# Kernel tuning notes

Hardware: AMD Instinct MI355X
Metric: run time of the kernel (lower is better)

## Reference

```python
import jax, jax.numpy as jnp
import numpy as np

NUM_HEADS = 16


def setup_inputs() -> dict:
    key = jax.random.key(0)
    ks = jax.random.split(key, 9)
    B, S, D = 2, 2048, 1024
    scale = 1.0 / np.sqrt(D)
    return {
        "hidden_states": jax.random.normal(ks[0], (B, S, D), dtype=jnp.float32),
        "Wq": jax.random.normal(ks[1], (D, D), dtype=jnp.float32) * scale,
        "bq": jnp.zeros((D,), dtype=jnp.float32),
        "Wk": jax.random.normal(ks[2], (D, D), dtype=jnp.float32) * scale,
        "bk": jnp.zeros((D,), dtype=jnp.float32),
        "Wv": jax.random.normal(ks[3], (D, D), dtype=jnp.float32) * scale,
        "bv": jnp.zeros((D,), dtype=jnp.float32),
        "Wo": jax.random.normal(ks[4], (D, D), dtype=jnp.float32) * scale,
        "bo": jnp.zeros((D,), dtype=jnp.float32),
    }


def reference(hidden_states, Wq, bq, Wk, bk, Wv, bv, Wo, bo):
    B, S, D = hidden_states.shape
    H = NUM_HEADS
    hd = D // H
    # q/k/v projections (torch Linear uses x @ W.T + b)
    q = hidden_states @ Wq.T + bq
    k = hidden_states @ Wk.T + bk
    v = hidden_states @ Wv.T + bv
    # split heads: b s (h d) -> b h s d
    q = q.reshape(B, S, H, hd)
    k = k.reshape(B, S, H, hd)
    v = v.reshape(B, S, H, hd)
    # scaled dot-product attention (non-causal, no mask)
    scale = 1.0 / jnp.sqrt(jnp.asarray(hd, dtype=q.dtype))
    scores = jnp.einsum("bqhd,bkhd->bhqk", q, k) * scale
    probs = jax.nn.softmax(scores, axis=-1)
    attn = jnp.einsum("bhqk,bkhd->bqhd", probs, v)
    # merge heads and output projection
    attn = attn.reshape(B, S, D)
    return attn @ Wo.T + bo
```

## Files before the change

### kernel.cpp

```cpp
#include <hip/hip_runtime.h>

typedef short bf16x8 __attribute__((ext_vector_type(8)));
typedef short bf16x4 __attribute__((ext_vector_type(4)));
typedef float f32x4 __attribute__((ext_vector_type(4)));
typedef float float4v __attribute__((ext_vector_type(4)));
typedef unsigned short u16x8 __attribute__((ext_vector_type(8)));
typedef unsigned short u16x4 __attribute__((ext_vector_type(4)));

#define GLL16(g, l_) __builtin_amdgcn_global_load_lds( \
    (const __attribute__((address_space(1))) unsigned int*)(g), \
    (__attribute__((address_space(3))) unsigned int*)(l_), 16, 0, 0)

__device__ __forceinline__ unsigned short f2bf(float x) {
  unsigned u = __float_as_uint(x);
  u += 0x7fff + ((u >> 16) & 1);
  return (unsigned short)(u >> 16);
}

__device__ __forceinline__ unsigned cvtpk_bf16(float a, float b) {
  unsigned r;
  asm("v_cvt_pk_bf16_f32 %0, %1, %2" : "=v"(r) : "v"(a), "v"(b));
  return r;
}

__global__ __launch_bounds__(256) void cast_all_kernel(
    const float* __restrict__ X, const float* __restrict__ Wq,
    const float* __restrict__ Wk, const float* __restrict__ Wv,
    const float* __restrict__ Wo,
    unsigned short* __restrict__ Xb, unsigned short* __restrict__ Wb) {
  int bx = blockIdx.x;
  const float* src; unsigned short* dst; int rel;
  if (bx < 2048) { src = X; dst = Xb; rel = bx; }
  else {
    int wi = (bx - 2048) >> 9; rel = (bx - 2048) & 511;
    src = (wi == 0) ? Wq : (wi == 1) ? Wk : (wi == 2) ? Wv : Wo;
    dst = Wb + ((size_t)wi << 20);
  }
  size_t o = (size_t)rel * 2048 + (size_t)threadIdx.x * 8;
  const float4v* s4 = (const float4v*)(src + o);
  float4v v0 = s4[0], v1 = s4[1];
  u16x8 r;
  r[0]=f2bf(v0[0]); r[1]=f2bf(v0[1]); r[2]=f2bf(v0[2]); r[3]=f2bf(v0[3]);
  r[4]=f2bf(v1[0]); r[5]=f2bf(v1[1]); r[6]=f2bf(v1[2]); r[7]=f2bf(v1[3]);
  *(u16x8*)(dst + o) = r;
}

__device__ __forceinline__ void gemm_core_128(
    const unsigned short* __restrict__ A, const unsigned short* __restrict__ Bt,
    int m0, int n0, int K,
    unsigned short* lA, unsigned short* lB, f32x4 acc[4][4]) {
  const int t = threadIdx.x;
  const int l = t & 63;
  const int wr = t >> 7, wc = (t >> 6) & 1;
  const int srow = t >> 3, scol = (t & 7) * 8;
  const int l15 = l & 15, lhi = l >> 4;
  for (int kt = 0; kt < K; kt += 64) {
#pragma unroll
    for (int p = 0; p < 4; ++p) {
      GLL16(A  + (size_t)(m0 + p * 32 + srow) * K + kt + scol, lA + (p * 32 + srow) * 64 + scol);
      GLL16(Bt + (size_t)(n0 + p * 32 + srow) * K + kt + scol, lB + (p * 32 + srow) * 64 + scol);
    }
    asm volatile("s_waitcnt vmcnt(0)" ::: "memory");
    __syncthreads();
#pragma unroll
    for (int ks = 0; ks < 2; ++ks) {
      bf16x8 af[4], bfr[4];
#pragma unroll
      for (int i = 0; i < 4; ++i) {
        af[i]  = *(const bf16x8*)(lA + (wr * 64 + i * 16 + l15) * 64 + ks * 32 + lhi * 8);
        bfr[i] = *(const bf16x8*)(lB + (wc * 64 + i * 16 + l15) * 64 + ks * 32 + lhi * 8);
      }
#pragma unroll
      for (int i = 0; i < 4; ++i)
#pragma unroll
        for (int j = 0; j < 4; ++j)
          acc[i][j] = __builtin_amdgcn_mfma_f32_16x16x32_bf16(af[i], bfr[j], acc[i][j], 0, 0, 0);
    }
    __syncthreads();
  }
}

__global__ __launch_bounds__(512, 1) void qkv_gemm256_kernel(
    const unsigned short* __restrict__ Xb, const unsigned short* __restrict__ Wb,
    const float* __restrict__ bq, const float* __restrict__ bk, const float* __restrict__ bv,
    unsigned short* __restrict__ Q, unsigned short* __restrict__ Kd,
    unsigned short* __restrict__ Vt, float qscale) {
  __shared__ __align__(16) unsigned short lds[2][2][256 * 64];
  const int bx0 = blockIdx.x;
  const int bx = (bx0 & 7) * 24 + (bx0 >> 3);
  const int mb = bx / 12, nb = bx % 12;
  const int t = threadIdx.x, l = t & 63;
  const int wm = (t >> 6) >> 2, wn = (t >> 6) & 3;
  const int l15 = l & 15, lhi = l >> 4, sw7 = l15 & 7;

  const unsigned short* Ag = Xb + (size_t)(mb * 256) * 1024;
  const unsigned short* Bg = Wb + (size_t)(nb * 256) * 1024;

  const int slc = (t & 7) ^ ((t >> 3) & 7);
#define STAGE256(kt_, ba_, bb_)                                                  \
  {                                                                              \
    _Pragma("unroll")                                                            \
    for (int i_ = 0; i_ < 4; ++i_) {                                             \
      const int srow = (t >> 3) + i_ * 64;                                       \
      GLL16(Ag + (size_t)srow * 1024 + (kt_) + slc * 8, (ba_) + (srow * 8 + (t & 7)) * 8); \
      GLL16(Bg + (size_t)srow * 1024 + (kt_) + slc * 8, (bb_) + (srow * 8 + (t & 7)) * 8); \
    }                                                                            \
  }
#define RD256(base_, rowbase_) \
  (*(const bf16x8*)((const char*)(base_) + ((rowbase_) + l15) * 128 + ((KS256 * 4 + lhi) ^ sw7) * 16))

  f32x4 acc[8][4];
#pragma unroll
  for (int mi = 0; mi < 8; ++mi)
#pragma unroll
    for (int ni = 0; ni < 4; ++ni)
#pragma unroll
      for (int r0 = 0; r0 < 4; ++r0) acc[mi][ni][r0] = 0.f;

  STAGE256(0, &lds[0][0][0], &lds[0][1][0]);
  asm volatile("s_waitcnt vmcnt(0)" ::: "memory");
  __builtin_amdgcn_s_barrier();

  int cur = 0;
  for (int kt = 0; kt < 1024; kt += 64) {
    const unsigned short* bA = &lds[cur][0][0];
    const unsigned short* bB = &lds[cur][1][0];
    if (kt + 64 < 1024) STAGE256(kt + 64, &lds[cur ^ 1][0][0], &lds[cur ^ 1][1][0]);

    bf16x8 af[4][2], b0[2][2], b1[2][2];
#pragma unroll
    for (int ks = 0; ks < 2; ++ks) {
      const int KS256 = ks;
#pragma unroll
      for (int mi = 0; mi < 4; ++mi) af[mi][ks] = RD256(bA, wm * 128 + mi * 16);
#pragma unroll
      for (int ni = 0; ni < 2; ++ni) b0[ni][ks] = RD256(bB, wn * 64 + ni * 16);
    }
    __builtin_amdgcn_s_setprio(1);
#pragma unroll
    for (int mi = 0; mi < 4; ++mi)
#pragma unroll
      for (int ni = 0; ni < 2; ++ni)
#pragma unroll
        for (int ks = 0; ks < 2; ++ks)
          acc[mi][ni] = __builtin_amdgcn_mfma_f32_16x16x32_bf16(af[mi][ks], b0[ni][ks], acc[mi][ni], 0, 0, 0);
    __builtin_amdgcn_s_setprio(0);
    __builtin_amdgcn_s_barrier();

#pragma unroll
    for (int ks = 0; ks < 2; ++ks) {
      const int KS256 = ks;
#pragma unroll
      for (int ni = 0; ni < 2; ++ni) b1[ni][ks] = RD256(bB, wn * 64 + (ni + 2) * 16);
    }
    __builtin_amdgcn_s_setprio(1);
#pragma unroll
    for (int mi = 0; mi < 4; ++mi)
#pragma unroll
      for (int ni = 0; ni < 2; ++ni)
#pragma unroll
        for (int ks = 0; ks < 2; ++ks)
          acc[mi][ni + 2] = __builtin_amdgcn_mfma_f32_16x16x32_bf16(af[mi][ks], b1[ni][ks], acc[mi][ni + 2], 0, 0, 0);
    __builtin_amdgcn_s_setprio(0);
    __builtin_amdgcn_s_barrier();

#pragma unroll
    for (int ks = 0; ks < 2; ++ks) {
      const int KS256 = ks;
#pragma unroll
      for (int mi = 0; mi < 4; ++mi) af[mi][ks] = RD256(bA, wm * 128 + (mi + 4) * 16);
    }
    __builtin_amdgcn_s_setprio(1);
#pragma unroll
    for (int mi = 0; mi < 4; ++mi)
#pragma unroll
      for (int ni = 0; ni < 2; ++ni)
#pragma unroll
        for (int ks = 0; ks < 2; ++ks)
          acc[mi + 4][ni] = __builtin_amdgcn_mfma_f32_16x16x32_bf16(af[mi][ks], b0[ni][ks], acc[mi + 4][ni], 0, 0, 0);
    __builtin_amdgcn_s_setprio(0);
    __builtin_amdgcn_s_barrier();

    __builtin_amdgcn_s_setprio(1);
#pragma unroll
    for (int mi = 0; mi < 4; ++mi)
#pragma unroll
      for (int ni = 0; ni < 2; ++ni)
#pragma unroll
        for (int ks = 0; ks < 2; ++ks)
          acc[mi + 4][ni + 2] = __builtin_amdgcn_mfma_f32_16x16x32_bf16(af[mi][ks], b1[ni][ks], acc[mi + 4][ni + 2], 0, 0, 0);
    __builtin_amdgcn_s_setprio(0);
    asm volatile("s_waitcnt vmcnt(0)" ::: "memory");
    __builtin_amdgcn_s_barrier();
    cur ^= 1;
  }
#undef STAGE256
#undef RD256

  const int kind = nb >> 2;
  const float* bias = (kind == 0) ? bq : (kind == 1) ? bk : bv;
#pragma unroll
  for (int mi = 0; mi < 8; ++mi)
#pragma unroll
    for (int ni = 0; ni < 4; ++ni) {
      int gm0 = mb * 256 + wm * 128 + mi * 16 + lhi * 4;
      int gn = nb * 256 + wn * 64 + ni * 16 + l15;
      int gnk = gn & 1023;
      float bb_ = bias[gnk];
      if (kind == 2) {
        int h = gnk >> 6, d = gnk & 63;
        int batch = gm0 >> 11, s = gm0 & 2047;
        u16x4 pk;
#pragma unroll
        for (int r0 = 0; r0 < 4; ++r0) pk[r0] = f2bf(acc[mi][ni][r0] + bb_);
        *(u16x4*)(Vt + ((size_t)(batch * 16 + h) * 64 + d) * 2048 + s) = pk;
      } else if (kind == 0) {
#pragma unroll
        for (int r0 = 0; r0 < 4; ++r0)
          Q[(size_t)(gm0 + r0) * 1024 + gnk] = f2bf((acc[mi][ni][r0] + bb_) * qscale);
      } else {
#pragma unroll
        for (int r0 = 0; r0 < 4; ++r0)
          Kd[(size_t)(gm0 + r0) * 1024 + gnk] = f2bf(acc[mi][ni][r0] + bb_);
      }
    }
}

__global__ __launch_bounds__(256, 3) void attn_kernel(
    const unsigned short* __restrict__ Q, const unsigned short* __restrict__ Kd,
    const unsigned short* __restrict__ Vt, unsigned short* __restrict__ Ao) {
  __shared__ __align__(16) unsigned short lKV[3][8192];
  const int bx0 = blockIdx.x;
  const int bx = (bx0 & 7) * 64 + (bx0 >> 3);
  const int bh = bx >> 4, qb = bx & 15;
  const int b = bh >> 4, h = bh & 15;
  const int t = threadIdx.x, l = t & 63;
  const int l15 = l & 15, lhi = l >> 4;
  const int q0 = b * 2048 + qb * 128 + (t >> 6) * 32;
  const unsigned short* Qp = Q + (size_t)q0 * 1024 + h * 64;
  const unsigned short* Kp = Kd + (size_t)b * 2048 * 1024 + h * 64;
  const unsigned short* Vp = Vt + (size_t)bh * 64 * 2048;

  bf16x8 qa[2][2];
#pragma unroll
  for (int rf = 0; rf < 2; ++rf)
#pragma unroll
    for (int ks = 0; ks < 2; ++ks)
      qa[rf][ks] = *(const bf16x8*)(Qp + (size_t)(rf * 16 + l15) * 1024 + ks * 32 + lhi * 8);

  f32x4 acc[2][4];
  float lsum[2];
#pragma unroll
  for (int rf = 0; rf < 2; ++rf) {
    lsum[rf] = 0.f;
#pragma unroll
    for (int j = 0; j < 4; ++j)
#pragma unroll
      for (int r0 = 0; r0 < 4; ++r0) acc[rf][j][r0] = 0.f;
  }

#define STAGE_KV(kb_, buf_)                                                   \
  {                                                                           \
    { int j = t;       int row = j >> 3, lch = (j & 7) ^ (row & 7);           \
      GLL16(Kp + (size_t)((kb_) + row) * 1024 + lch * 8, (buf_) + j * 8); }   \
    { int j = t + 256; int row = j >> 3, lch = (j & 7) ^ (row & 7);           \
      GLL16(Kp + (size_t)((kb_) + row) * 1024 + lch * 8, (buf_) + j * 8); }   \
    { int j = t;       int row = j >> 3, lch = (j & 7) ^ (row & 7);           \
      GLL16(Vp + (size_t)row * 2048 + (kb_) + lch * 8, (buf_) + 4096 + j * 8); } \
    { int j = t + 256; int row = j >> 3, lch = (j & 7) ^ (row & 7);           \
      GLL16(Vp + (size_t)row * 2048 + (kb_) + lch * 8, (buf_) + 4096 + j * 8); } \
  }

  unsigned short* L0 = &lKV[0][0];
  STAGE_KV(0, L0);
  STAGE_KV(64, L0 + 8192);

  for (int ti = 0; ti < 32; ++ti) {
    const unsigned short* bK = L0 + (ti % 3) * 8192;
    const unsigned short* bV = bK + 4096;
    if (ti < 30) {
      unsigned short* nbuf = L0 + ((ti + 2) % 3) * 8192;
      STAGE_KV((ti + 2) * 64, nbuf);
      asm volatile("s_waitcnt vmcnt(8)" ::: "memory");
    } else if (ti == 30) {
      asm volatile("s_waitcnt vmcnt(4)" ::: "memory");
    } else {
      asm volatile("s_waitcnt vmcnt(0)" ::: "memory");
    }
    __builtin_amdgcn_s_barrier();

    f32x4 st[2][4];
#pragma unroll
    for (int rf = 0; rf < 2; ++rf)
#pragma unroll
      for (int cf = 0; cf < 4; ++cf)
#pragma unroll
        for (int r0 = 0; r0 < 4; ++r0) st[rf][cf][r0] = 0.f;
    __builtin_amdgcn_s_setprio(1);
#pragma unroll
    for (int ks = 0; ks < 2; ++ks) {
      bf16x8 kfr[4];
#pragma unroll
      for (int cf = 0; cf < 4; ++cf)
        kfr[cf] = *(const bf16x8*)(bK + (cf * 16 + l15) * 64 + (((ks * 4 + lhi) ^ (l15 & 7)) << 3));
#pragma unroll
      for (int rf = 0; rf < 2; ++rf)
#pragma unroll
        for (int cf = 0; cf < 4; ++cf)
          st[rf][cf] = __builtin_amdgcn_mfma_f32_16x16x32_bf16(kfr[cf], qa[rf][ks], st[rf][cf], 0, 0, 0);
    }
    __builtin_amdgcn_s_setprio(0);

    unsigned pk[2][4][2];
#pragma unroll
    for (int rf = 0; rf < 2; ++rf)
#pragma unroll
      for (int cf = 0; cf < 4; ++cf) {
        float p0 = __builtin_amdgcn_exp2f(st[rf][cf][0]);
        float p1 = __builtin_amdgcn_exp2f(st[rf][cf][1]);
        float p2 = __builtin_amdgcn_exp2f(st[rf][cf][2]);
        float p3 = __builtin_amdgcn_exp2f(st[rf][cf][3]);
        lsum[rf] += (p0 + p1) + (p2 + p3);
        pk[rf][cf][0] = cvtpk_bf16(p0, p1);
        pk[rf][cf][1] = cvtpk_bf16(p2, p3);
      }

    __builtin_amdgcn_s_setprio(1);
#pragma unroll
    for (int ks = 0; ks < 2; ++ks) {
      bf16x8 pa[2];
#pragma unroll
      for (int rf = 0; rf < 2; ++rf) {
        union { unsigned u[4]; bf16x8 v; } pu;
        pu.u[0] = pk[rf][2 * ks][0];     pu.u[1] = pk[rf][2 * ks][1];
        pu.u[2] = pk[rf][2 * ks + 1][0]; pu.u[3] = pk[rf][2 * ks + 1][1];
        pa[rf] = pu.v;
      }
#pragma unroll
      for (int df = 0; df < 4; ++df) {
        const int row = df * 16 + l15;
        const char* vb = (const char*)bV + row * 128;
        const int sw = (row & 7) << 4;
        bf16x4 lo = *(const bf16x4*)(vb + ((ks * 64 + lhi * 8) ^ sw));
        bf16x4 hi = *(const bf16x4*)(vb + ((ks * 64 + 32 + lhi * 8) ^ sw));
        bf16x8 vf = {lo[0], lo[1], lo[2], lo[3], hi[0], hi[1], hi[2], hi[3]};
#pragma unroll
        for (int rf = 0; rf < 2; ++rf)
          acc[rf][df] = __builtin_amdgcn_mfma_f32_16x16x32_bf16(pa[rf], vf, acc[rf][df], 0, 0, 0);
      }
    }
    __builtin_amdgcn_s_setprio(0);

    __builtin_amdgcn_s_barrier();
  }
#undef STAGE_KV

#pragma unroll
  for (int rf = 0; rf < 2; ++rf) {
    lsum[rf] += __shfl_xor(lsum[rf], 16);
    lsum[rf] += __shfl_xor(lsum[rf], 32);
  }
  float rn[2][4];
#pragma unroll
  for (int rf = 0; rf < 2; ++rf)
#pragma unroll
    for (int r0 = 0; r0 < 4; ++r0)
      rn[rf][r0] = 1.0f / __shfl(lsum[rf], lhi * 4 + r0);
#pragma unroll
  for (int rf = 0; rf < 2; ++rf)
#pragma unroll
    for (int r0 = 0; r0 < 4; ++r0) {
      int grow = q0 + rf * 16 + lhi * 4 + r0;
#pragma unroll
      for (int df = 0; df < 4; ++df) {
        int gcol = h * 64 + df * 16 + l15;
        Ao[(size_t)grow * 1024 + gcol] = f2bf(acc[rf][df][r0] * rn[rf][r0]);
      }
    }
}

__global__ __launch_bounds__(256) void out_gemm_kernel(
    const unsigned short* __restrict__ Ab, const unsigned short* __restrict__ Wob,
    const float* __restrict__ bo, float* __restrict__ Out) {
  __shared__ __align__(16) unsigned short lA[128 * 64];
  __shared__ __align__(16) unsigned short lB[128 * 64];
  const int bx0 = blockIdx.x;
  const int bx = (bx0 & 7) * 32 + (bx0 >> 3);
  const int mb = bx >> 3, nb = bx & 7;
  f32x4 acc[4][4];
#pragma unroll
  for (int i = 0; i < 4; ++i)
#pragma unroll
    for (int j = 0; j < 4; ++j)
#pragma unroll
      for (int r0 = 0; r0 < 4; ++r0) acc[i][j][r0] = 0.f;
  gemm_core_128(Ab, Wob, mb * 128, nb * 128, 1024, lA, lB, acc);
  const int t = threadIdx.x, l = t & 63;
  const int wr = t >> 7, wc = (t >> 6) & 1;
  const int l15 = l & 15, lhi = l >> 4;
#pragma unroll
  for (int i = 0; i < 4; ++i)
#pragma unroll
    for (int j = 0; j < 4; ++j) {
      int gn = nb * 128 + wc * 64 + j * 16 + l15;
      float bb_ = bo[gn];
      int gm0 = mb * 128 + wr * 64 + i * 16 + lhi * 4;
#pragma unroll
      for (int r0 = 0; r0 < 4; ++r0)
        Out[(size_t)(gm0 + r0) * 1024 + gn] = acc[i][j][r0] + bb_;
    }
}

extern "C" void kernel_launch(void* const* d_in, const int* in_sizes, int n_in,
                              void* d_out, int out_size, void* d_ws, size_t ws_size,
                              hipStream_t stream) {
  const float* X  = (const float*)d_in[0];
  const float* Wq = (const float*)d_in[1];
  const float* bq = (const float*)d_in[2];
  const float* Wk = (const float*)d_in[3];
  const float* bk = (const float*)d_in[4];
  const float* Wv = (const float*)d_in[5];
  const float* bv = (const float*)d_in[6];
  const float* Wo = (const float*)d_in[7];
  const float* bo = (const float*)d_in[8];
  char* ws = (char*)d_ws;
  unsigned short* Xb = (unsigned short*)(ws);
  unsigned short* Wb = (unsigned short*)(ws + ((size_t)8  << 20));
  unsigned short* Qb = (unsigned short*)(ws + ((size_t)16 << 20));
  unsigned short* Kb = (unsigned short*)(ws + ((size_t)24 << 20));
  unsigned short* Vt = (unsigned short*)(ws + ((size_t)32 << 20));
  unsigned short* Ab = (unsigned short*)(ws + ((size_t)40 << 20));

  const float qscale = 1.4426950408889634f / 8.0f;

  cast_all_kernel<<<4096, 256, 0, stream>>>(X, Wq, Wk, Wv, Wo, Xb, Wb);
  qkv_gemm256_kernel<<<192, 512, 0, stream>>>(Xb, Wb, bq, bk, bv, Qb, Kb, Vt, qscale);
  attn_kernel<<<512, 256, 0, stream>>>(Qb, Kb, Vt, Ab);
  out_gemm_kernel<<<256, 256, 0, stream>>>(Ab, Wb + ((size_t)3 << 20), bo, (float*)d_out);
}
```

Measured before the change: 118.3 us.

## Double attention and output GEMM waves per block, add XOR-swizzled LDS tiles

The attention kernel moves from 256 to 512 threads per block, so each wave owns 16 query rows instead of 32. Each thread now issues one K and one V load per stage, and the vmcnt waits are adjusted to match. The output GEMM is inlined with 512 threads (8 waves, each with a 32x64 sub-tile) and gains an XOR swizzle on its LDS staging to avoid bank conflicts. The aim is more waves for latency hiding and fewer LDS conflicts. The cost is that each wave reuses every loaded K/V fragment for fewer MFMAs, and a larger block may limit residency.

Result: faster. 114.4 us (-3.3%).

```diff
diff --git a/kernel.cpp b/kernel.cpp
--- a/kernel.cpp
+++ b/kernel.cpp
@@ -45,41 +45,6 @@
   *(u16x8*)(dst + o) = r;
 }
 
-__device__ __forceinline__ void gemm_core_128(
-    const unsigned short* __restrict__ A, const unsigned short* __restrict__ Bt,
-    int m0, int n0, int K,
-    unsigned short* lA, unsigned short* lB, f32x4 acc[4][4]) {
-  const int t = threadIdx.x;
-  const int l = t & 63;
-  const int wr = t >> 7, wc = (t >> 6) & 1;
-  const int srow = t >> 3, scol = (t & 7) * 8;
-  const int l15 = l & 15, lhi = l >> 4;
-  for (int kt = 0; kt < K; kt += 64) {
-#pragma unroll
-    for (int p = 0; p < 4; ++p) {
-      GLL16(A  + (size_t)(m0 + p * 32 + srow) * K + kt + scol, lA + (p * 32 + srow) * 64 + scol);
-      GLL16(Bt + (size_t)(n0 + p * 32 + srow) * K + kt + scol, lB + (p * 32 + srow) * 64 + scol);
-    }
-    asm volatile("s_waitcnt vmcnt(0)" ::: "memory");
-    __syncthreads();
-#pragma unroll
-    for (int ks = 0; ks < 2; ++ks) {
-      bf16x8 af[4], bfr[4];
-#pragma unroll
-      for (int i = 0; i < 4; ++i) {
-        af[i]  = *(const bf16x8*)(lA + (wr * 64 + i * 16 + l15) * 64 + ks * 32 + lhi * 8);
-        bfr[i] = *(const bf16x8*)(lB + (wc * 64 + i * 16 + l15) * 64 + ks * 32 + lhi * 8);
-      }
-#pragma unroll
-      for (int i = 0; i < 4; ++i)
-#pragma unroll
-        for (int j = 0; j < 4; ++j)
-          acc[i][j] = __builtin_amdgcn_mfma_f32_16x16x32_bf16(af[i], bfr[j], acc[i][j], 0, 0, 0);
-    }
-    __syncthreads();
-  }
-}
-
 __global__ __launch_bounds__(512, 1) void qkv_gemm256_kernel(
     const unsigned short* __restrict__ Xb, const unsigned short* __restrict__ Wb,
     const float* __restrict__ bq, const float* __restrict__ bk, const float* __restrict__ bv,
@@ -226,7 +191,7 @@
     }
 }
 
-__global__ __launch_bounds__(256, 3) void attn_kernel(
+__global__ __launch_bounds__(512, 4) void attn_kernel(
     const unsigned short* __restrict__ Q, const unsigned short* __restrict__ Kd,
     const unsigned short* __restrict__ Vt, unsigned short* __restrict__ Ao) {
   __shared__ __align__(16) unsigned short lKV[3][8192];
@@ -234,41 +199,30 @@
   const int bx = (bx0 & 7) * 64 + (bx0 >> 3);
   const int bh = bx >> 4, qb = bx & 15;
   const int b = bh >> 4, h = bh & 15;
-  const int t = threadIdx.x, l = t & 63;
+  const int t = threadIdx.x, l = t & 63, w = t >> 6;
   const int l15 = l & 15, lhi = l >> 4;
-  const int q0 = b * 2048 + qb * 128 + (t >> 6) * 32;
+  const int q0 = b * 2048 + qb * 128 + w * 16;
   const unsigned short* Qp = Q + (size_t)q0 * 1024 + h * 64;
   const unsigned short* Kp = Kd + (size_t)b * 2048 * 1024 + h * 64;
   const unsigned short* Vp = Vt + (size_t)bh * 64 * 2048;
 
-  bf16x8 qa[2][2];
-#pragma unroll
-  for (int rf = 0; rf < 2; ++rf)
-#pragma unroll
-    for (int ks = 0; ks < 2; ++ks)
-      qa[rf][ks] = *(const bf16x8*)(Qp + (size_t)(rf * 16 + l15) * 1024 + ks * 32 + lhi * 8);
-
-  f32x4 acc[2][4];
-  float lsum[2];
-#pragma unroll
-  for (int rf = 0; rf < 2; ++rf) {
-    lsum[rf] = 0.f;
-#pragma unroll
-    for (int j = 0; j < 4; ++j)
-#pragma unroll
-      for (int r0 = 0; r0 < 4; ++r0) acc[rf][j][r0] = 0.f;
-  }
-
-#define STAGE_KV(kb_, buf_)                                                   \
-  {                                                                           \
-    { int j = t;       int row = j >> 3, lch = (j & 7) ^ (row & 7);           \
-      GLL16(Kp + (size_t)((kb_) + row) * 1024 + lch * 8, (buf_) + j * 8); }   \
-    { int j = t + 256; int row = j >> 3, lch = (j & 7) ^ (row & 7);           \
-      GLL16(Kp + (size_t)((kb_) + row) * 1024 + lch * 8, (buf_) + j * 8); }   \
-    { int j = t;       int row = j >> 3, lch = (j & 7) ^ (row & 7);           \
-      GLL16(Vp + (size_t)row * 2048 + (kb_) + lch * 8, (buf_) + 4096 + j * 8); } \
-    { int j = t + 256; int row = j >> 3, lch = (j & 7) ^ (row & 7);           \
-      GLL16(Vp + (size_t)row * 2048 + (kb_) + lch * 8, (buf_) + 4096 + j * 8); } \
+  bf16x8 qa[2];
+#pragma unroll
+  for (int ks = 0; ks < 2; ++ks)
+    qa[ks] = *(const bf16x8*)(Qp + (size_t)l15 * 1024 + ks * 32 + lhi * 8);
+
+  f32x4 acc[4];
+  float lsum = 0.f;
+#pragma unroll
+  for (int j = 0; j < 4; ++j)
+#pragma unroll
+    for (int r0 = 0; r0 < 4; ++r0) acc[j][r0] = 0.f;
+
+#define STAGE_KV(kb_, buf_)                                                      \
+  {                                                                              \
+    int row = t >> 3, lch = (t & 7) ^ (row & 7);                                 \
+    GLL16(Kp + (size_t)((kb_) + row) * 1024 + lch * 8, (buf_) + t * 8);          \
+    GLL16(Vp + (size_t)row * 2048 + (kb_) + lch * 8, (buf_) + 4096 + t * 8);     \
   }
 
   unsigned short* L0 = &lKV[0][0];
@@ -281,21 +235,19 @@
     if (ti < 30) {
       unsigned short* nbuf = L0 + ((ti + 2) % 3) * 8192;
       STAGE_KV((ti + 2) * 64, nbuf);
-      asm volatile("s_waitcnt vmcnt(8)" ::: "memory");
+      asm volatile("s_waitcnt vmcnt(4)" ::: "memory");
     } else if (ti == 30) {
-      asm volatile("s_waitcnt vmcnt(4)" ::: "memory");
+      asm volatile("s_waitcnt vmcnt(2)" ::: "memory");
     } else {
       asm volatile("s_waitcnt vmcnt(0)" ::: "memory");
     }
     __builtin_amdgcn_s_barrier();
 
-    f32x4 st[2][4];
-#pragma unroll
-    for (int rf = 0; rf < 2; ++rf)
-#pragma unroll
-      for (int cf = 0; cf < 4; ++cf)
-#pragma unroll
-        for (int r0 = 0; r0 < 4; ++r0) st[rf][cf][r0] = 0.f;
+    f32x4 st[4];
+#pragma unroll
+    for (int cf = 0; cf < 4; ++cf)
+#pragma unroll
+      for (int r0 = 0; r0 < 4; ++r0) st[cf][r0] = 0.f;
     __builtin_amdgcn_s_setprio(1);
 #pragma unroll
     for (int ks = 0; ks < 2; ++ks) {
@@ -304,38 +256,30 @@
       for (int cf = 0; cf < 4; ++cf)
         kfr[cf] = *(const bf16x8*)(bK + (cf * 16 + l15) * 64 + (((ks * 4 + lhi) ^ (l15 & 7)) << 3));
 #pragma unroll
-      for (int rf = 0; rf < 2; ++rf)
-#pragma unroll
-        for (int cf = 0; cf < 4; ++cf)
-          st[rf][cf] = __builtin_amdgcn_mfma_f32_16x16x32_bf16(kfr[cf], qa[rf][ks], st[rf][cf], 0, 0, 0);
-    }
-    __builtin_amdgcn_s_setprio(0);
-
-    unsigned pk[2][4][2];
-#pragma unroll
-    for (int rf = 0; rf < 2; ++rf)
-#pragma unroll
-      for (int cf = 0; cf < 4; ++cf) {
-        float p0 = __builtin_amdgcn_exp2f(st[rf][cf][0]);
-        float p1 = __builtin_amdgcn_exp2f(st[rf][cf][1]);
-        float p2 = __builtin_amdgcn_exp2f(st[rf][cf][2]);
-        float p3 = __builtin_amdgcn_exp2f(st[rf][cf][3]);
-        lsum[rf] += (p0 + p1) + (p2 + p3);
-        pk[rf][cf][0] = cvtpk_bf16(p0, p1);
-        pk[rf][cf][1] = cvtpk_bf16(p2, p3);
-      }
-
-    __builtin_amdgcn_s_setprio(1);
-#pragma unroll
-    for (int ks = 0; ks < 2; ++ks) {
-      bf16x8 pa[2];
-#pragma unroll
-      for (int rf = 0; rf < 2; ++rf) {
-        union { unsigned u[4]; bf16x8 v; } pu;
-        pu.u[0] = pk[rf][2 * ks][0];     pu.u[1] = pk[rf][2 * ks][1];
-        pu.u[2] = pk[rf][2 * ks + 1][0]; pu.u[3] = pk[rf][2 * ks + 1][1];
-        pa[rf] = pu.v;
-      }
+      for (int cf = 0; cf < 4; ++cf)
+        st[cf] = __builtin_amdgcn_mfma_f32_16x16x32_bf16(kfr[cf], qa[ks], st[cf], 0, 0, 0);
+    }
+    __builtin_amdgcn_s_setprio(0);
+
+    unsigned pk[4][2];
+#pragma unroll
+    for (int cf = 0; cf < 4; ++cf) {
+      float p0 = __builtin_amdgcn_exp2f(st[cf][0]);
+      float p1 = __builtin_amdgcn_exp2f(st[cf][1]);
+      float p2 = __builtin_amdgcn_exp2f(st[cf][2]);
+      float p3 = __builtin_amdgcn_exp2f(st[cf][3]);
+      lsum += (p0 + p1) + (p2 + p3);
+      pk[cf][0] = cvtpk_bf16(p0, p1);
+      pk[cf][1] = cvtpk_bf16(p2, p3);
+    }
+
+    __builtin_amdgcn_s_setprio(1);
+#pragma unroll
+    for (int ks = 0; ks < 2; ++ks) {
+      union { unsigned u[4]; bf16x8 v; } pu;
+      pu.u[0] = pk[2 * ks][0];     pu.u[1] = pk[2 * ks][1];
+      pu.u[2] = pk[2 * ks + 1][0]; pu.u[3] = pk[2 * ks + 1][1];
+      bf16x8 pa = pu.v;
 #pragma unroll
       for (int df = 0; df < 4; ++df) {
         const int row = df * 16 + l15;
@@ -344,9 +288,7 @@
         bf16x4 lo = *(const bf16x4*)(vb + ((ks * 64 + lhi * 8) ^ sw));
         bf16x4 hi = *(const bf16x4*)(vb + ((ks * 64 + 32 + lhi * 8) ^ sw));
         bf16x8 vf = {lo[0], lo[1], lo[2], lo[3], hi[0], hi[1], hi[2], hi[3]};
-#pragma unroll
-        for (int rf = 0; rf < 2; ++rf)
-          acc[rf][df] = __builtin_amdgcn_mfma_f32_16x16x32_bf16(pa[rf], vf, acc[rf][df], 0, 0, 0);
+        acc[df] = __builtin_amdgcn_mfma_f32_16x16x32_bf16(pa, vf, acc[df], 0, 0, 0);
       }
     }
     __builtin_amdgcn_s_setprio(0);
@@ -355,31 +297,24 @@
   }
 #undef STAGE_KV
 
-#pragma unroll
-  for (int rf = 0; rf < 2; ++rf) {
-    lsum[rf] += __shfl_xor(lsum[rf], 16);
-    lsum[rf] += __shfl_xor(lsum[rf], 32);
-  }
-  float rn[2][4];
-#pragma unroll
-  for (int rf = 0; rf < 2; ++rf)
-#pragma unroll
-    for (int r0 = 0; r0 < 4; ++r0)
-      rn[rf][r0] = 1.0f / __shfl(lsum[rf], lhi * 4 + r0);
-#pragma unroll
-  for (int rf = 0; rf < 2; ++rf)
-#pragma unroll
-    for (int r0 = 0; r0 < 4; ++r0) {
-      int grow = q0 + rf * 16 + lhi * 4 + r0;
-#pragma unroll
-      for (int df = 0; df < 4; ++df) {
-        int gcol = h * 64 + df * 16 + l15;
-        Ao[(size_t)grow * 1024 + gcol] = f2bf(acc[rf][df][r0] * rn[rf][r0]);
-      }
-    }
-}
-
-__global__ __launch_bounds__(256) void out_gemm_kernel(
+  lsum += __shfl_xor(lsum, 16);
+  lsum += __shfl_xor(lsum, 32);
+  float rn[4];
+#pragma unroll
+  for (int r0 = 0; r0 < 4; ++r0)
+    rn[r0] = 1.0f / __shfl(lsum, lhi * 4 + r0);
+#pragma unroll
+  for (int r0 = 0; r0 < 4; ++r0) {
+    int grow = q0 + lhi * 4 + r0;
+#pragma unroll
+    for (int df = 0; df < 4; ++df) {
+      int gcol = h * 64 + df * 16 + l15;
+      Ao[(size_t)grow * 1024 + gcol] = f2bf(acc[df][r0] * rn[r0]);
+    }
+  }
+}
+
+__global__ __launch_bounds__(512) void out_gemm_kernel(
     const unsigned short* __restrict__ Ab, const unsigned short* __restrict__ Wob,
     const float* __restrict__ bo, float* __restrict__ Out) {
   __shared__ __align__(16) unsigned short lA[128 * 64];
@@ -387,24 +322,56 @@
   const int bx0 = blockIdx.x;
   const int bx = (bx0 & 7) * 32 + (bx0 >> 3);
   const int mb = bx >> 3, nb = bx & 7;
-  f32x4 acc[4][4];
-#pragma unroll
-  for (int i = 0; i < 4; ++i)
+  const int t = threadIdx.x, l = t & 63, w = t >> 6;
+  const int wr = w >> 1, wc = w & 1;
+  const int l15 = l & 15, lhi = l >> 4, sw7 = l15 & 7;
+  const unsigned short* Ag = Ab + (size_t)(mb * 128) * 1024;
+  const unsigned short* Bg = Wob + (size_t)(nb * 128) * 1024;
+
+  f32x4 acc[2][4];
+#pragma unroll
+  for (int i = 0; i < 2; ++i)
 #pragma unroll
     for (int j = 0; j < 4; ++j)
 #pragma unroll
       for (int r0 = 0; r0 < 4; ++r0) acc[i][j][r0] = 0.f;
-  gemm_core_128(Ab, Wob, mb * 128, nb * 128, 1024, lA, lB, acc);
-  const int t = threadIdx.x, l = t & 63;
-  const int wr = t >> 7, wc = (t >> 6) & 1;
-  const int l15 = l & 15, lhi = l >> 4;
-#pragma unroll
-  for (int i = 0; i < 4; ++i)
+
+  for (int kt = 0; kt < 1024; kt += 64) {
+    {
+      int row = t >> 3, lch = (t & 7) ^ (row & 7);
+      GLL16(Ag + (size_t)row * 1024 + kt + lch * 8, lA + t * 8);
+      GLL16(Bg + (size_t)row * 1024 + kt + lch * 8, lB + t * 8);
+      int j2 = t + 512, row2 = j2 >> 3, lch2 = (j2 & 7) ^ (row2 & 7);
+      GLL16(Ag + (size_t)row2 * 1024 + kt + lch2 * 8, lA + j2 * 8);
+      GLL16(Bg + (size_t)row2 * 1024 + kt + lch2 * 8, lB + j2 * 8);
+    }
+    asm volatile("s_waitcnt vmcnt(0)" ::: "memory");
+    __syncthreads();
+#pragma unroll
+    for (int ks = 0; ks < 2; ++ks) {
+      bf16x8 af[2], bfr[4];
+#pragma unroll
+      for (int i = 0; i < 2; ++i)
+        af[i] = *(const bf16x8*)(lA + (wr * 32 + i * 16 + l15) * 64 + (((ks * 4 + lhi) ^ sw7) << 3));
+#pragma unroll
+      for (int j = 0; j < 4; ++j)
+        bfr[j] = *(const bf16x8*)(lB + (wc * 64 + j * 16 + l15) * 64 + (((ks * 4 + lhi) ^ sw7) << 3));
+#pragma unroll
+      for (int i = 0; i < 2; ++i)
+#pragma unroll
+        for (int j = 0; j < 4; ++j)
+          acc[i][j] = __builtin_amdgcn_mfma_f32_16x16x32_bf16(af[i], bfr[j], acc[i][j], 0, 0, 0);
+    }
+    __syncthreads();
+  }
+
+#pragma unroll
+  for (int i = 0; i < 2; ++i)
 #pragma unroll
     for (int j = 0; j < 4; ++j) {
       int gn = nb * 128 + wc * 64 + j * 16 + l15;
       float bb_ = bo[gn];
-      int gm0 = mb * 128 + wr * 64 + i * 16 + lhi * 4;
+      int gm0 = mb * 128 + wr * 32 + i * 16 + lhi * 4;
 #pragma unroll
       for (int r0 = 0; r0 < 4; ++r0)
         Out[(size_t)(gm0 + r0) * 1024 + gn] = acc[i][j][r0] + bb_;
@@ -435,6 +402,6 @@
 
   cast_all_kernel<<<4096, 256, 0, stream>>>(X, Wq, Wk, Wv, Wo, Xb, Wb);
   qkv_gemm256_kernel<<<192, 512, 0, stream>>>(Xb, Wb, bq, bk, bv, Qb, Kb, Vt, qscale);
-  attn_kernel<<<512, 256, 0, stream>>>(Qb, Kb, Vt, Ab);
-  out_gemm_kernel<<<256, 256, 0, stream>>>(Ab, Wb + ((size_t)3 << 20), bo, (float*)d_out);
-}
+  attn_kernel<<<512, 512, 0, stream>>>(Qb, Kb, Vt, Ab);
+  out_gemm_kernel<<<256, 512, 0, stream>>>(Ab, Wb + ((size_t)3 << 20), bo, (float*)d_out);
+}
```
